# Performance work log

Measured on AMD Instinct MI355X. Metric: run time of the kernel, lower is better.

## Reference

```python
import jax, jax.numpy as jnp
import numpy as np

W, L, K, N = 32, 64, 512, 64


def setup_inputs() -> dict:
    key = jax.random.key(0)
    k0, k1, k2, k3 = jax.random.split(key, 4)
    # 0/1 spin states stored as float, matching torch.randint(0, 2, ..., dtype=float32)
    states = jax.random.randint(k0, (W, L, K, N), 0, 2).astype(jnp.float32)
    Q = jax.random.normal(k1, (W, N, N), dtype=jnp.float32)
    # inverse temperatures, ascending (standard parallel-tempering ladder)
    beta = jnp.sort(jax.random.uniform(k2, (L,), minval=0.1, maxval=2.0, dtype=jnp.float32))
    # uniform draws replacing torch.rand_like(delta) in exchange()
    u = jax.random.uniform(k3, (W, L - 1, K), dtype=jnp.float32)
    return {"states": states, "Q": Q, "beta": beta, "u": u}


def reference(states, Q, beta, u):
    """Temperer.exchange(): energies then masked replica swap.

    Returns (energies (W,L,K) before exchange, new states (W,L,K,N)).
    """
    # energy: einsum('wlki,wij,wlkj->wlk') done as one GEMM + elementwise reduce
    sQ = jnp.einsum('wlki,wij->wlkj', states, Q)          # (W,L,K,N)
    energies = jnp.einsum('wlkj,wlkj->wlk', sQ, states)   # (W,L,K)

    dbeta = (beta[1:] - beta[:-1])[None, :, None]          # (1,L-1,1)
    delta = (energies[:, 1:] - energies[:, :-1]) * dbeta   # (W,L-1,K)
    mask = (u < jnp.exp(delta)).astype(states.dtype)[..., None]  # (W,L-1,K,1)

    left = states[:, :-1]
    right = states[:, 1:]
    # replicate torch's sequential overlapping slice assignments exactly
    new = states.at[:, :-1].set(mask * right + (1.0 - mask) * left)
    new = new.at[:, 1:].set(mask * left + (1.0 - mask) * right)
    return energies, new
```

## Files before the change

kernel.cpp:

```cpp
#include <hip/hip_runtime.h>
#include <math.h>

#define PW 32
#define PL 64
#define PK 512
#define PN 64

typedef int   v4i __attribute__((ext_vector_type(4)));
typedef float v4f __attribute__((ext_vector_type(4)));


__global__ __launch_bounds__(256) void pack_kernel(
    const float* __restrict__ states, unsigned long long* __restrict__ pmask)
{
    const int lane = threadIdx.x & 63;
    const long wave = ((long)blockIdx.x * blockDim.x + threadIdx.x) >> 6;
    const long vb = wave * 16;

    unsigned long long pm = 0;
#pragma unroll
    for (int it = 0; it < 4; ++it) {
        const v4f* gp = (const v4f*)(states + (vb + it * 4) * PN);
        const v4f f = gp[lane];
        const unsigned long long m0 = __ballot(f.x != 0.0f);
        const unsigned long long m1 = __ballot(f.y != 0.0f);
        const unsigned long long m2 = __ballot(f.z != 0.0f);
        const unsigned long long m3 = __ballot(f.w != 0.0f);
        unsigned long long mm[4];
#pragma unroll
        for (int vv = 0; vv < 4; ++vv) {
            mm[vv] = ((m0 >> (vv * 16)) & 0xFFFFull)
                   | (((m1 >> (vv * 16)) & 0xFFFFull) << 16)
                   | (((m2 >> (vv * 16)) & 0xFFFFull) << 32)
                   | (((m3 >> (vv * 16)) & 0xFFFFull) << 48);
        }
        const unsigned long long s01 = (lane & 1) ? mm[1] : mm[0];
        const unsigned long long s23 = (lane & 1) ? mm[3] : mm[2];
        const unsigned long long sel = (lane & 2) ? s23 : s01;
        pm = ((lane >> 2) == it) ? sel : pm;
    }
    if (lane < 16) pmask[vb + lane] = pm;
}

constexpr int ITERS_PER_WAVE = 4;

__global__ __launch_bounds__(256) void energies_kernel(
    const unsigned long long* __restrict__ pmask, const float* __restrict__ Q,
    float* __restrict__ e_out, double* __restrict__ e64)
{
    __shared__ alignas(16) signed char Afrag[16 * 64 * 16];

    const int tid  = threadIdx.x;
    const int lane = tid & 63;
    const int wv   = tid >> 6;
    const int w    = blockIdx.x >> 6;
    const int blk  = blockIdx.x & 63;

    const float* Qw = Q + w * PN * PN;
    for (int e = tid; e < PN * PN; e += 256) {
        const int i = e >> 6, j = e & 63;
        long long R = llrint((double)Qw[e] * 268435456.0);
        const int h = i & 3, b = i >> 2;
        const int frag_lane = (h << 4) | (j & 15);
        const int jt = j >> 4;
#pragma unroll
        for (int k = 0; k < 4; ++k) {
            const signed char d = (signed char)(R & 0xFF);
            R = (R - d) >> 8;
            Afrag[((k * 4 + jt) * 64 + frag_lane) * 16 + b] = d;
        }
    }
    __syncthreads();

    const v4i* Af = (const v4i*)Afrag;

    const long vw_base = (long)w * (PL * PK)
                       + (long)(blk * 4 + wv) * (32 * ITERS_PER_WAVE);
    const int h = lane >> 4;

    for (int t = 0; t < ITERS_PER_WAVE; ++t) {
        const long vbase = vw_base + (long)t * 32;

        const unsigned long long pmA = pmask[vbase + (lane & 15)];
        const unsigned long long pmB = pmask[vbase + 16 + (lane & 15)];

        const unsigned int bA = (unsigned int)(pmA >> (h * 16)) & 0xFFFFu;
        const unsigned int bB = (unsigned int)(pmB >> (h * 16)) & 0xFFFFu;
        v4i BA, BB;
#pragma unroll
        for (int q = 0; q < 4; ++q) {
            BA[q] = (int)((((bA >> (4 * q)) & 0xFu) * 0x00204081u) & 0x01010101u);
            BB[q] = (int)((((bB >> (4 * q)) & 0xFu) * 0x01010101u >> 0) & 0x01010101u);
        }
#pragma unroll
        for (int q = 0; q < 4; ++q)
            BB[q] = (int)((((bB >> (4 * q)) & 0xFu) * 0x00204081u) & 0x01010101u);

        unsigned int xA[4], xB[4];
#pragma unroll
        for (int r = 0; r < 4; ++r) {
            xA[r] = (unsigned int)(pmA >> (r * 16 + h)) & 0x1111u;
            xB[r] = (unsigned int)(pmB >> (r * 16 + h)) & 0x1111u;
        }

        long long accA = 0, accB = 0;
#pragma unroll
        for (int k = 0; k < 4; ++k) {
            v4i A0 = Af[(k * 4 + 0) * 64 + lane];
            v4i A1 = Af[(k * 4 + 1) * 64 + lane];
            v4i A2 = Af[(k * 4 + 2) * 64 + lane];
            v4i A3 = Af[(k * 4 + 3) * 64 + lane];
            v4i CA0 = {0,0,0,0}, CA1 = {0,0,0,0}, CA2 = {0,0,0,0}, CA3 = {0,0,0,0};
            v4i CB0 = {0,0,0,0}, CB1 = {0,0,0,0}, CB2 = {0,0,0,0}, CB3 = {0,0,0,0};
            asm("s_nop 1\n\t"
                "v_mfma_i32_16x16x64_i8 %0, %8, %12, %0\n\t"
                "v_mfma_i32_16x16x64_i8 %4, %8, %13, %4\n\t"
                "v_mfma_i32_16x16x64_i8 %1, %9, %12, %1\n\t"
                "v_mfma_i32_16x16x64_i8 %5, %9, %13, %5\n\t"
                "v_mfma_i32_16x16x64_i8 %2, %10, %12, %2\n\t"
                "v_mfma_i32_16x16x64_i8 %6, %10, %13, %6\n\t"
                "v_mfma_i32_16x16x64_i8 %3, %11, %12, %3\n\t"
                "v_mfma_i32_16x16x64_i8 %7, %11, %13, %7\n\t"
                "s_nop 7\n\t"
                "s_nop 7"
                : "+v"(CA0), "+v"(CA1), "+v"(CA2), "+v"(CA3),
                  "+v"(CB0), "+v"(CB1), "+v"(CB2), "+v"(CB3)
                : "v"(A0), "v"(A1), "v"(A2), "v"(A3), "v"(BA), "v"(BB));
            int akA = 0, akB = 0;
#pragma unroll
            for (int r = 0; r < 4; ++r) {
                akA += ((xA[r] >> 0)  & 1) * CA0[r];
                akA += ((xA[r] >> 4)  & 1) * CA1[r];
                akA += ((xA[r] >> 8)  & 1) * CA2[r];
                akA += ((xA[r] >> 12) & 1) * CA3[r];
                akB += ((xB[r] >> 0)  & 1) * CB0[r];
                akB += ((xB[r] >> 4)  & 1) * CB1[r];
                akB += ((xB[r] >> 8)  & 1) * CB2[r];
                akB += ((xB[r] >> 12) & 1) * CB3[r];
            }
            accA += (long long)akA << (8 * k);
            accB += (long long)akB << (8 * k);
        }

        accA += __shfl_xor(accA, 16, 64);
        accA += __shfl_xor(accA, 32, 64);
        accB += __shfl_xor(accB, 16, 64);
        accB += __shfl_xor(accB, 32, 64);

        if (lane < 16) {
            const double eA = (double)accA * 0x1p-28;
            const double eB = (double)accB * 0x1p-28;
            e64[vbase + lane]        = eA;
            e_out[vbase + lane]      = (float)eA;
            e64[vbase + 16 + lane]   = eB;
            e_out[vbase + 16 + lane] = (float)eB;
        }
    }
}

__global__ __launch_bounds__(256) void mask_kernel(
    const double* __restrict__ e64, const float* __restrict__ beta,
    const float* __restrict__ u, unsigned char* __restrict__ mask)
{
    const int idx = blockIdx.x * blockDim.x + threadIdx.x;
    if (idx >= PW * (PL - 1) * PK) return;
    const int k = idx % PK;
    const int m = (idx / PK) % (PL - 1);
    const int w = idx / (PK * (PL - 1));
    const long e1 = ((long)w * PL + m) * PK + k;
    const double db = (double)beta[m + 1] - (double)beta[m];
    const double delta = (e64[e1 + PK] - e64[e1]) * db;
    mask[idx] = ((double)u[idx] < exp(delta)) ? 1 : 0;
}

__global__ __launch_bounds__(256) void swap_kernel(
    const float* __restrict__ states, const unsigned char* __restrict__ mask,
    float* __restrict__ out)
{
    const long rowBase = (long)blockIdx.x * 32;
    const int w  = (int)(rowBase >> 15);
    const int l  = (int)((rowBase >> 9) & 63);
    const int k0 = (int)(rowBase & 511);

    const int tid = threadIdx.x;
    const int r  = tid >> 3;
    const int j4 = tid & 7;
    const int k  = k0 + r;

    const int ml = (l == 0) ? 0 : (l - 1);
    const unsigned char mk = mask[((long)w * (PL - 1) + ml) * PK + k];
    int sl;
    if (l == 0) sl = mk ? 1 : 0;
    else        sl = mk ? (l - 1) : l;

    const float4* srcp = (const float4*)(states + (((long)w * PL + sl) * PK + k) * PN);
    float4*       dstp = (float4*)(out + (rowBase + r) * PN);
    dstp[j4]     = srcp[j4];
    dstp[j4 + 8] = srcp[j4 + 8];
}

extern "C" void kernel_launch(void* const* d_in, const int* in_sizes, int n_in,
                              void* d_out, int out_size, void* d_ws, size_t ws_size,
                              hipStream_t stream) {
    const float* states = (const float*)d_in[0];
    const float* Q      = (const float*)d_in[1];
    const float* beta   = (const float*)d_in[2];
    const float* u      = (const float*)d_in[3];

    float* e_out      = (float*)d_out;
    float* new_states = (float*)d_out + (long)PW * PL * PK;

    const long NV = (long)PW * PL * PK;
    double* e64 = (double*)d_ws;
    unsigned long long* pmask = (unsigned long long*)((char*)d_ws + 8 * NV);
    unsigned char* mask = (unsigned char*)d_ws + 16 * NV;

    pack_kernel<<<16384, 256, 0, stream>>>(states, pmask);

    energies_kernel<<<2048, 256, 0, stream>>>(pmask, Q, e_out, e64);

    const int nmask = PW * (PL - 1) * PK;
    mask_kernel<<<(nmask + 255) / 256, 256, 0, stream>>>(e64, beta, u, mask);

    swap_kernel<<<32768, 256, 0, stream>>>(states, mask, new_states);
}
```

Before: 526.2 us.

## Fuse bit-packing into energies kernel and mask into swap using packed states

The standalone pack kernel goes away: the energies kernel now reads the float states directly, ballots them into 64-bit bitmasks, writes those masks out and uses them for the MFMA. The mask kernel is folded into the swap kernel, which computes the accept decision per row and rebuilds the output floats from the packed bitmask instead of re-reading the full float states. This cuts two launches and replaces a second full read of the states with small bitmask reads. In exchange the energies kernel does more global loading per wave, and the swap kernel repeats the exp and accept logic once per row.

```diff
diff --git a/kernel.cpp b/kernel.cpp
--- a/kernel.cpp
+++ b/kernel.cpp
@@ -10,43 +10,12 @@
 typedef float v4f __attribute__((ext_vector_type(4)));
 
 
-__global__ __launch_bounds__(256) void pack_kernel(
-    const float* __restrict__ states, unsigned long long* __restrict__ pmask)
-{
-    const int lane = threadIdx.x & 63;
-    const long wave = ((long)blockIdx.x * blockDim.x + threadIdx.x) >> 6;
-    const long vb = wave * 16;
-
-    unsigned long long pm = 0;
-#pragma unroll
-    for (int it = 0; it < 4; ++it) {
-        const v4f* gp = (const v4f*)(states + (vb + it * 4) * PN);
-        const v4f f = gp[lane];
-        const unsigned long long m0 = __ballot(f.x != 0.0f);
-        const unsigned long long m1 = __ballot(f.y != 0.0f);
-        const unsigned long long m2 = __ballot(f.z != 0.0f);
-        const unsigned long long m3 = __ballot(f.w != 0.0f);
-        unsigned long long mm[4];
-#pragma unroll
-        for (int vv = 0; vv < 4; ++vv) {
-            mm[vv] = ((m0 >> (vv * 16)) & 0xFFFFull)
-                   | (((m1 >> (vv * 16)) & 0xFFFFull) << 16)
-                   | (((m2 >> (vv * 16)) & 0xFFFFull) << 32)
-                   | (((m3 >> (vv * 16)) & 0xFFFFull) << 48);
-        }
-        const unsigned long long s01 = (lane & 1) ? mm[1] : mm[0];
-        const unsigned long long s23 = (lane & 1) ? mm[3] : mm[2];
-        const unsigned long long sel = (lane & 2) ? s23 : s01;
-        pm = ((lane >> 2) == it) ? sel : pm;
-    }
-    if (lane < 16) pmask[vb + lane] = pm;
-}
-
 constexpr int ITERS_PER_WAVE = 4;
 
 __global__ __launch_bounds__(256) void energies_kernel(
-    const unsigned long long* __restrict__ pmask, const float* __restrict__ Q,
-    float* __restrict__ e_out, double* __restrict__ e64)
+    const float* __restrict__ states, const float* __restrict__ Q,
+    float* __restrict__ e_out, double* __restrict__ e64,
+    unsigned long long* __restrict__ pmask)
 {
     __shared__ alignas(16) signed char Afrag[16 * 64 * 16];
 
@@ -76,13 +45,32 @@
 
     const long vw_base = (long)w * (PL * PK)
                        + (long)(blk * 4 + wv) * (32 * ITERS_PER_WAVE);
-    const int h = lane >> 4;
+    const int h   = lane >> 4;
+    const int g16 = (lane & 3) * 16;
+    const int itA = (lane & 15) >> 2;
+    const int itO = (lane & 31) >> 2;
 
     for (int t = 0; t < ITERS_PER_WAVE; ++t) {
         const long vbase = vw_base + (long)t * 32;
 
-        const unsigned long long pmA = pmask[vbase + (lane & 15)];
-        const unsigned long long pmB = pmask[vbase + 16 + (lane & 15)];
+        unsigned long long pmA = 0, pmB = 0, pmO = 0;
+#pragma unroll
+        for (int it = 0; it < 8; ++it) {
+            const v4f f = ((const v4f*)(states + (vbase + it * 4) * PN))[lane];
+            const unsigned long long m0 = __ballot(f.x != 0.0f);
+            const unsigned long long m1 = __ballot(f.y != 0.0f);
+            const unsigned long long m2 = __ballot(f.z != 0.0f);
+            const unsigned long long m3 = __ballot(f.w != 0.0f);
+            const unsigned long long cand =
+                  ((m0 >> g16) & 0xFFFFull)
+                | (((m1 >> g16) & 0xFFFFull) << 16)
+                | (((m2 >> g16) & 0xFFFFull) << 32)
+                | (((m3 >> g16) & 0xFFFFull) << 48);
+            pmA = (it == itA)     ? cand : pmA;
+            pmB = (it == itA + 4) ? cand : pmB;
+            pmO = (it == itO)     ? cand : pmO;
+        }
+        if (lane < 32) pmask[vbase + lane] = pmO;
 
         const unsigned int bA = (unsigned int)(pmA >> (h * 16)) & 0xFFFFu;
         const unsigned int bB = (unsigned int)(pmB >> (h * 16)) & 0xFFFFu;
@@ -90,11 +78,8 @@
 #pragma unroll
         for (int q = 0; q < 4; ++q) {
             BA[q] = (int)((((bA >> (4 * q)) & 0xFu) * 0x00204081u) & 0x01010101u);
-            BB[q] = (int)((((bB >> (4 * q)) & 0xFu) * 0x01010101u >> 0) & 0x01010101u);
-        }
-#pragma unroll
-        for (int q = 0; q < 4; ++q)
             BB[q] = (int)((((bB >> (4 * q)) & 0xFu) * 0x00204081u) & 0x01010101u);
+        }
 
         unsigned int xA[4], xB[4];
 #pragma unroll
@@ -158,45 +143,40 @@
     }
 }
 
-__global__ __launch_bounds__(256) void mask_kernel(
-    const double* __restrict__ e64, const float* __restrict__ beta,
-    const float* __restrict__ u, unsigned char* __restrict__ mask)
-{
-    const int idx = blockIdx.x * blockDim.x + threadIdx.x;
-    if (idx >= PW * (PL - 1) * PK) return;
-    const int k = idx % PK;
-    const int m = (idx / PK) % (PL - 1);
-    const int w = idx / (PK * (PL - 1));
-    const long e1 = ((long)w * PL + m) * PK + k;
-    const double db = (double)beta[m + 1] - (double)beta[m];
-    const double delta = (e64[e1 + PK] - e64[e1]) * db;
-    mask[idx] = ((double)u[idx] < exp(delta)) ? 1 : 0;
-}
-
 __global__ __launch_bounds__(256) void swap_kernel(
-    const float* __restrict__ states, const unsigned char* __restrict__ mask,
+    const unsigned long long* __restrict__ pmask,
+    const double* __restrict__ e64,
+    const float* __restrict__ beta, const float* __restrict__ u,
     float* __restrict__ out)
 {
-    const long rowBase = (long)blockIdx.x * 32;
-    const int w  = (int)(rowBase >> 15);
-    const int l  = (int)((rowBase >> 9) & 63);
-    const int k0 = (int)(rowBase & 511);
-
+    const long row0 = (long)blockIdx.x * 16;
     const int tid = threadIdx.x;
-    const int r  = tid >> 3;
-    const int j4 = tid & 7;
-    const int k  = k0 + r;
-
-    const int ml = (l == 0) ? 0 : (l - 1);
-    const unsigned char mk = mask[((long)w * (PL - 1) + ml) * PK + k];
-    int sl;
-    if (l == 0) sl = mk ? 1 : 0;
-    else        sl = mk ? (l - 1) : l;
-
-    const float4* srcp = (const float4*)(states + (((long)w * PL + sl) * PK + k) * PN);
-    float4*       dstp = (float4*)(out + (rowBase + r) * PN);
-    dstp[j4]     = srcp[j4];
-    dstp[j4 + 8] = srcp[j4 + 8];
+    const long row = row0 + (tid >> 4);
+    const int e = tid & 15;
+    const int w = (int)(row >> 15);
+    const int l = (int)((row >> 9) & 63);
+    const int k = (int)(row & 511);
+
+    long src;
+    if (l == 0) {
+        const double db = (double)beta[1] - (double)beta[0];
+        const double delta = (e64[row + PK] - e64[row]) * db;
+        const float uv = u[(long)w * (PL - 1) * PK + k];
+        src = row + (((double)uv < exp(delta)) ? PK : 0);
+    } else {
+        const double db = (double)beta[l] - (double)beta[l - 1];
+        const double delta = (e64[row] - e64[row - PK]) * db;
+        const float uv = u[((long)w * (PL - 1) + (l - 1)) * PK + k];
+        src = row - (((double)uv < exp(delta)) ? PK : 0);
+    }
+
+    const unsigned long long pm = pmask[src];
+    v4f f;
+    f.x = ((pm >> e)        & 1) ? 1.0f : 0.0f;
+    f.y = ((pm >> (16 + e)) & 1) ? 1.0f : 0.0f;
+    f.z = ((pm >> (32 + e)) & 1) ? 1.0f : 0.0f;
+    f.w = ((pm >> (48 + e)) & 1) ? 1.0f : 0.0f;
+    ((v4f*)(out + row * PN))[e] = f;
 }
 
 extern "C" void kernel_launch(void* const* d_in, const int* in_sizes, int n_in,
@@ -213,14 +193,8 @@
     const long NV = (long)PW * PL * PK;
     double* e64 = (double*)d_ws;
     unsigned long long* pmask = (unsigned long long*)((char*)d_ws + 8 * NV);
-    unsigned char* mask = (unsigned char*)d_ws + 16 * NV;
-
-    pack_kernel<<<16384, 256, 0, stream>>>(states, pmask);
-
-    energies_kernel<<<2048, 256, 0, stream>>>(pmask, Q, e_out, e64);
-
-    const int nmask = PW * (PL - 1) * PK;
-    mask_kernel<<<(nmask + 255) / 256, 256, 0, stream>>>(e64, beta, u, mask);
-
-    swap_kernel<<<32768, 256, 0, stream>>>(states, mask, new_states);
+
+    energies_kernel<<<2048, 256, 0, stream>>>(states, Q, e_out, e64, pmask);
+
+    swap_kernel<<<65536, 256, 0, stream>>>(pmask, e64, beta, u, new_states);
 }
```

Measured after the change: 513.5 us. -2.4%, faster.
